# Optimization experiments

Measured on AMD Instinct MI355X. Metric: run time of the kernel, lower is better.

The kernel has to match this reference:

```python
import jax, jax.numpy as jnp
import numpy as np

NEG_INF = -1e30  # masked-softmax sentinel (exactly reproduces index_select+softmax)


def _pool(lbh, mask, scorer_w, layer_w):
    # lbh: [L, T, H]; mask: [T] bool selecting the pooled positions.
    # Masked softmax over positions == softmax over index_select'ed positions.
    scores = jnp.einsum('lth,ch->ltc', lbh, scorer_w)            # [L, T, C]
    scores = jnp.where(mask[None, :, None], scores, NEG_INF)
    attn = jax.nn.softmax(scores, axis=1)                        # zero at masked pos
    pooled = jnp.einsum('lth,ltc->lch', lbh, attn)               # [L, C, H]
    combined = jnp.einsum('l,lch->ch', layer_w, pooled)          # [C, H]
    return combined.reshape(-1)                                  # [C*H]


def reference(hidden_states, input_ids, layer_logits, scorer_w, hte_token_id, d_token_ids, window):
    layers = hidden_states[1:]                                   # [L, B, T, H]
    L, B, T, H = layers.shape
    ar = jnp.arange(T)
    layer_w = jax.nn.softmax(layer_logits)                       # [L]

    # HTE window mask: first occurrence of hte_token_id (else T-1), pos..pos+window
    is_hte = input_ids == hte_token_id                           # [B, T]
    pos = jnp.where(is_hte.any(-1), jnp.argmax(is_hte, axis=-1), T - 1)  # [B]
    win_mask = (ar[None, :] >= pos[:, None]) & (ar[None, :] <= pos[:, None] + window)

    # Descriptor mask: any position matching any d_token_id; fallback = position 0
    desc = (input_ids[:, :, None] == d_token_ids[None, None, :]).any(-1)  # [B, T]
    desc_mask = jnp.where(desc.any(-1, keepdims=True), desc, ar[None, :] == 0)

    layers_b = jnp.transpose(layers, (1, 0, 2, 3))               # [B, L, T, H]
    pool = jax.vmap(lambda lbh, m: _pool(lbh, m, scorer_w, layer_w))
    pooled_hte = pool(layers_b, win_mask)                        # [B, C*H]
    pooled_desc = pool(layers_b, desc_mask)                      # [B, C*H]
    return jnp.concatenate([pooled_hte, pooled_desc], axis=-1)   # [B, 2*C*H]


def setup_inputs() -> dict:
    key = jax.random.key(0)
    k_h, k_ids, k_ll, k_w = jax.random.split(key, 4)
    NUM_LAYERS, B, T, H, C, VOCAB = 12, 8, 2048, 768, 4, 512
    return {
        'hidden_states': jax.random.normal(k_h, (NUM_LAYERS + 1, B, T, H), dtype=jnp.float32),
        'input_ids': jax.random.randint(k_ids, (B, T), 0, VOCAB, dtype=jnp.int64),
        'layer_logits': jax.random.normal(k_ll, (NUM_LAYERS,), dtype=jnp.float32),
        'scorer_w': jax.random.normal(k_w, (C, H), dtype=jnp.float32) * 0.02,
        'hte_token_id': 5,
        'd_token_ids': jnp.arange(3, dtype=jnp.int64),
        'window': 4,
    }
```

## Files before the change

kernel.cpp:

```cpp
#include <hip/hip_runtime.h>

#define TPB 256
#define CMAX 8

__global__ void mha_agg_kernel(const float* __restrict__ hidden,
                               const int* __restrict__ ids,
                               const float* __restrict__ layer_logits,
                               const float* __restrict__ scorer_w,
                               const int* __restrict__ hte_id_p,
                               const int* __restrict__ d_tok,
                               const int* __restrict__ window_p,
                               float* __restrict__ out,
                               int L, int B, int T, int H, int C, int ND)
{
    const int bid  = blockIdx.x;
    const int l    = bid % L;
    const int m    = (bid / L) & 1;
    const int b    = bid / (2 * L);
    const int tid  = threadIdx.x;
    const int wave = tid >> 6;
    const int lane = tid & 63;

    extern __shared__ unsigned char smem_raw[];
    unsigned short* s_sel    = (unsigned short*)smem_raw;
    float*          s_scores = (float*)(smem_raw + ((2 * T + 15) & ~15));
    float*          s_sw     = s_scores + (size_t)T * C;
    int*            s_misc   = (int*)(s_sw + (size_t)C * H);

    if (tid == 0) { s_misc[0] = T; s_misc[1] = 0; }
    for (int i = tid; i < C * H; i += TPB) s_sw[i] = scorer_w[i];
    __syncthreads();

    const int* idrow = ids + (size_t)b * T;
    if (m == 0) {
        const int hte = hte_id_p[0];
        for (int t = tid; t < T; t += TPB)
            if (idrow[t] == hte) atomicMin(&s_misc[0], t);
        __syncthreads();
        if (tid == 0) {
            int pos = s_misc[0]; if (pos >= T) pos = T - 1;
            int win = window_p[0];
            int hi = pos + win; if (hi > T - 1) hi = T - 1;
            int n = hi - pos + 1;
            for (int i = 0; i < n; i++) s_sel[i] = (unsigned short)(pos + i);
            s_misc[1] = n;
        }
    } else {
        int dt[CMAX];
        for (int d = 0; d < ND; d++) dt[d] = d_tok[d];
        for (int t = tid; t < T; t += TPB) {
            int v = idrow[t];
            bool hit = false;
            for (int d = 0; d < ND; d++) hit = hit || (v == dt[d]);
            if (hit) { int idx = atomicAdd(&s_misc[1], 1); s_sel[idx] = (unsigned short)t; }
        }
        __syncthreads();
        if (tid == 0 && s_misc[1] == 0) { s_sel[0] = 0; s_misc[1] = 1; }
    }
    __syncthreads();
    const int n = s_misc[1];

    float mx = -3.402823466e38f;
    for (int j = 0; j < L; j++) mx = fmaxf(mx, layer_logits[j]);
    float den = 0.f;
    for (int j = 0; j < L; j++) den += expf(layer_logits[j] - mx);
    const float lwl = expf(layer_logits[l] - mx) / den;

    const float* base = hidden + ((size_t)(l + 1) * B + b) * (size_t)T * H;

    for (int i = wave; i < n; i += TPB / 64) {
        const float* row = base + (size_t)s_sel[i] * H;
        float p[CMAX];
        for (int c = 0; c < C; c++) p[c] = 0.f;
        for (int h = lane; h < H; h += 64) {
            float v = row[h];
            for (int c = 0; c < C; c++) p[c] += v * s_sw[c * H + h];
        }
        for (int off = 32; off; off >>= 1)
            for (int c = 0; c < C; c++) p[c] += __shfl_down(p[c], off);
        if (lane == 0)
            for (int c = 0; c < C; c++) s_scores[i * C + c] = p[c];
    }
    __syncthreads();

    for (int c = wave; c < C; c += TPB / 64) {
        float smax = -3.402823466e38f;
        for (int i = lane; i < n; i += 64) smax = fmaxf(smax, s_scores[i * C + c]);
        for (int off = 32; off; off >>= 1) smax = fmaxf(smax, __shfl_xor(smax, off));
        float ssum = 0.f;
        for (int i = lane; i < n; i += 64) {
            float e = expf(s_scores[i * C + c] - smax);
            s_scores[i * C + c] = e;
            ssum += e;
        }
        for (int off = 32; off; off >>= 1) ssum += __shfl_xor(ssum, off);
        const float scale = lwl / ssum;
        for (int i = lane; i < n; i += 64) s_scores[i * C + c] *= scale;
    }
    __syncthreads();

    float* obase = out + ((size_t)b * 2 + m) * (size_t)C * H;
    for (int h = tid; h < H; h += TPB) {
        float a[CMAX];
        for (int c = 0; c < C; c++) a[c] = 0.f;
        for (int i = 0; i < n; i++) {
            float v = base[(size_t)s_sel[i] * H + h];
            for (int c = 0; c < C; c++) a[c] += s_scores[i * C + c] * v;
        }
        for (int c = 0; c < C; c++) atomicAdd(obase + c * H + h, a[c]);
    }
}

extern "C" void kernel_launch(void* const* d_in, const int* in_sizes, int n_in,
                              void* d_out, int out_size, void* d_ws, size_t ws_size,
                              hipStream_t stream) {
    const float* hidden = (const float*)d_in[0];
    const int*   ids    = (const int*)d_in[1];
    const float* ll     = (const float*)d_in[2];
    const float* sw     = (const float*)d_in[3];
    const int*   hte    = (const int*)d_in[4];
    const int*   dtok   = (const int*)d_in[5];
    const int*   win    = (const int*)d_in[6];
    float*       out    = (float*)d_out;

    const int L  = in_sizes[2];
    const int CH = in_sizes[3];
    const int B  = out_size / (2 * CH);
    const int T  = in_sizes[1] / B;
    const int H  = (int)((long long)in_sizes[0] / ((long long)(L + 1) * in_sizes[1]));
    const int C  = CH / H;
    const int ND = in_sizes[5];

    hipMemsetAsync(d_out, 0, (size_t)out_size * sizeof(float), stream);

    const size_t smem = (size_t)((2 * T + 15) & ~15)
                      + (size_t)T * C * sizeof(float)
                      + (size_t)CH * sizeof(float)
                      + 16;
    mha_agg_kernel<<<B * 2 * L, TPB, smem, stream>>>(hidden, ids, ll, sw, hte, dtok, win, out,
                                                     L, B, T, H, C, ND);
}
```

Measured before the change: 767.7 us.

## Parallelize over scorer heads instead of layers and drop atomics and memset

```diff
diff --git a/kernel.cpp b/kernel.cpp
--- a/kernel.cpp
+++ b/kernel.cpp
@@ -1,7 +1,8 @@
 #include <hip/hip_runtime.h>
 
 #define TPB 256
-#define CMAX 8
+#define NDMAX 8
+#define HREG 8
 
 __global__ void mha_agg_kernel(const float* __restrict__ hidden,
                                const int* __restrict__ ids,
@@ -14,21 +15,21 @@
                                int L, int B, int T, int H, int C, int ND)
 {
     const int bid  = blockIdx.x;
-    const int l    = bid % L;
-    const int m    = (bid / L) & 1;
-    const int b    = bid / (2 * L);
+    const int c    = bid % C;
+    const int m    = (bid / C) & 1;
+    const int b    = bid / (2 * C);
     const int tid  = threadIdx.x;
     const int wave = tid >> 6;
     const int lane = tid & 63;
 
-    extern __shared__ unsigned char smem_raw[];
-    unsigned short* s_sel    = (unsigned short*)smem_raw;
-    float*          s_scores = (float*)(smem_raw + ((2 * T + 15) & ~15));
-    float*          s_sw     = s_scores + (size_t)T * C;
-    int*            s_misc   = (int*)(s_sw + (size_t)C * H);
+    extern __shared__ unsigned char smem[];
+    unsigned short* s_sel  = (unsigned short*)smem;
+    float*          s_w    = (float*)(smem + ((2 * T + 15) & ~15));
+    float*          s_sc   = s_w + H;
+    int*            s_misc = (int*)(s_sc + T);
 
     if (tid == 0) { s_misc[0] = T; s_misc[1] = 0; }
-    for (int i = tid; i < C * H; i += TPB) s_sw[i] = scorer_w[i];
+    for (int h = tid; h < H; h += TPB) s_w[h] = scorer_w[(size_t)c * H + h];
     __syncthreads();
 
     const int* idrow = ids + (size_t)b * T;
@@ -41,18 +42,18 @@
             int pos = s_misc[0]; if (pos >= T) pos = T - 1;
             int win = window_p[0];
             int hi = pos + win; if (hi > T - 1) hi = T - 1;
-            int n = hi - pos + 1;
-            for (int i = 0; i < n; i++) s_sel[i] = (unsigned short)(pos + i);
-            s_misc[1] = n;
+            int nn = hi - pos + 1;
+            for (int i = 0; i < nn; i++) s_sel[i] = (unsigned short)(pos + i);
+            s_misc[1] = nn;
         }
     } else {
-        int dt[CMAX];
+        int dt[NDMAX];
         for (int d = 0; d < ND; d++) dt[d] = d_tok[d];
         for (int t = tid; t < T; t += TPB) {
             int v = idrow[t];
             bool hit = false;
             for (int d = 0; d < ND; d++) hit = hit || (v == dt[d]);
-            if (hit) { int idx = atomicAdd(&s_misc[1], 1); s_sel[idx] = (unsigned short)t; }
+            if (hit) { int k = atomicAdd(&s_misc[1], 1); s_sel[k] = (unsigned short)t; }
         }
         __syncthreads();
         if (tid == 0 && s_misc[1] == 0) { s_sel[0] = 0; s_misc[1] = 1; }
@@ -60,54 +61,49 @@
     __syncthreads();
     const int n = s_misc[1];
 
-    float mx = -3.402823466e38f;
-    for (int j = 0; j < L; j++) mx = fmaxf(mx, layer_logits[j]);
-    float den = 0.f;
-    for (int j = 0; j < L; j++) den += expf(layer_logits[j] - mx);
-    const float lwl = expf(layer_logits[l] - mx) / den;
+    float lmx = -3.402823466e38f;
+    for (int j = 0; j < L; j++) lmx = fmaxf(lmx, layer_logits[j]);
+    float lden = 0.f;
+    for (int j = 0; j < L; j++) lden += expf(layer_logits[j] - lmx);
 
-    const float* base = hidden + ((size_t)(l + 1) * B + b) * (size_t)T * H;
+    const int nh = (H + TPB - 1) / TPB;
+    float acc[HREG];
+    for (int k = 0; k < HREG; k++) acc[k] = 0.f;
 
-    for (int i = wave; i < n; i += TPB / 64) {
-        const float* row = base + (size_t)s_sel[i] * H;
-        float p[CMAX];
-        for (int c = 0; c < C; c++) p[c] = 0.f;
-        for (int h = lane; h < H; h += 64) {
-            float v = row[h];
-            for (int c = 0; c < C; c++) p[c] += v * s_sw[c * H + h];
+    for (int l = 0; l < L; l++) {
+        const float lwl = expf(layer_logits[l] - lmx) / lden;
+        const float* base = hidden + ((size_t)(l + 1) * B + b) * (size_t)T * H;
+
+        for (int i = wave; i < n; i += TPB / 64) {
+            const float* row = base + (size_t)s_sel[i] * H;
+            float p = 0.f;
+            for (int h = lane; h < H; h += 64) p += row[h] * s_w[h];
+            for (int off = 32; off; off >>= 1) p += __shfl_down(p, off);
+            if (lane == 0) s_sc[i] = p;
         }
-        for (int off = 32; off; off >>= 1)
-            for (int c = 0; c < C; c++) p[c] += __shfl_down(p[c], off);
-        if (lane == 0)
-            for (int c = 0; c < C; c++) s_scores[i * C + c] = p[c];
+        __syncthreads();
+
+        float smax = -3.402823466e38f;
+        for (int i = 0; i < n; i++) smax = fmaxf(smax, s_sc[i]);
+        float ssum = 0.f;
+        for (int i = 0; i < n; i++) ssum += expf(s_sc[i] - smax);
+        const float scale = lwl / ssum;
+
+        for (int i = 0; i < n; i++) {
+            const float wgt = expf(s_sc[i] - smax) * scale;
+            const float* row = base + (size_t)s_sel[i] * H;
+            for (int k = 0; k < nh; k++) {
+                int h = tid + k * TPB;
+                if (h < H) acc[k] += wgt * row[h];
+            }
+        }
+        __syncthreads();
     }
-    __syncthreads();
 
-    for (int c = wave; c < C; c += TPB / 64) {
-        float smax = -3.402823466e38f;
-        for (int i = lane; i < n; i += 64) smax = fmaxf(smax, s_scores[i * C + c]);
-        for (int off = 32; off; off >>= 1) smax = fmaxf(smax, __shfl_xor(smax, off));
-        float ssum = 0.f;
-        for (int i = lane; i < n; i += 64) {
-            float e = expf(s_scores[i * C + c] - smax);
-            s_scores[i * C + c] = e;
-            ssum += e;
-        }
-        for (int off = 32; off; off >>= 1) ssum += __shfl_xor(ssum, off);
-        const float scale = lwl / ssum;
-        for (int i = lane; i < n; i += 64) s_scores[i * C + c] *= scale;
-    }
-    __syncthreads();
-
-    float* obase = out + ((size_t)b * 2 + m) * (size_t)C * H;
-    for (int h = tid; h < H; h += TPB) {
-        float a[CMAX];
-        for (int c = 0; c < C; c++) a[c] = 0.f;
-        for (int i = 0; i < n; i++) {
-            float v = base[(size_t)s_sel[i] * H + h];
-            for (int c = 0; c < C; c++) a[c] += s_scores[i * C + c] * v;
-        }
-        for (int c = 0; c < C; c++) atomicAdd(obase + c * H + h, a[c]);
+    float* obase = out + (((size_t)b * 2 + m) * C + c) * (size_t)H;
+    for (int k = 0; k < nh; k++) {
+        int h = tid + k * TPB;
+        if (h < H) obase[h] = acc[k];
     }
 }
 
@@ -131,12 +127,10 @@
     const int C  = CH / H;
     const int ND = in_sizes[5];
 
-    hipMemsetAsync(d_out, 0, (size_t)out_size * sizeof(float), stream);
-
     const size_t smem = (size_t)((2 * T + 15) & ~15)
-                      + (size_t)T * C * sizeof(float)
-                      + (size_t)CH * sizeof(float)
+                      + (size_t)H * sizeof(float)
+                      + (size_t)T * sizeof(float)
                       + 16;
-    mha_agg_kernel<<<B * 2 * L, TPB, smem, stream>>>(hidden, ids, ll, sw, hte, dtok, win, out,
+    mha_agg_kernel<<<B * 2 * C, TPB, smem, stream>>>(hidden, ids, ll, sw, hte, dtok, win, out,
                                                      L, B, T, H, C, ND);
 }
```

New measurement: 1.063 ms. 38.5% more time.
